# Performance work log

Measured on AMD Instinct MI355X. Metric: run time of the kernel, lower is better.

## Reference

```python
import jax, jax.numpy as jnp
import numpy as np

N, F_IN, D, R, E = 50000, 128, 96, 2, 800000


def setup_inputs() -> dict:
    key = jax.random.key(0)
    ks = jax.random.split(key, 8)
    sc = lambda k, shape: jax.random.normal(k, shape, jnp.float32) * 0.05
    return {
        "x": jax.random.normal(ks[0], (N, F_IN), jnp.float32),
        "edge_index": jax.random.randint(ks[1], (2, E), 0, N),
        "edge_attr": jax.random.uniform(ks[2], (E, R), dtype=jnp.float32),
        # nn.Linear(F_IN, D)
        "Wf": sc(ks[3], (D, F_IN)),
        "bf": jnp.zeros((D,), jnp.float32),
        # RGCNConv: per-relation weights, root weight, bias
        "W": sc(ks[4], (R, D, D)),
        "root": sc(ks[5], (D, D)),
        "bias": jnp.zeros((D,), jnp.float32),
    }


def _rgcn_conv(h, src, dst, etype, W, root, bias):
    # PyG RGCNConv (no bases/blocks, aggr='mean'):
    #   out = x @ root + bias + sum_r mean_{edges of type r}(x[src]) @ W[r]
    msg = h[src]  # [E, D] gather
    out = h @ root + bias
    for r in range(R):
        w = (etype == r).astype(h.dtype)[:, None]  # [E, 1] relation mask
        s = jax.ops.segment_sum(msg * w, dst, num_segments=N)   # [N, D] scatter-add
        cnt = jax.ops.segment_sum(w, dst, num_segments=N)       # [N, 1]
        agg = s / jnp.maximum(cnt, 1.0)                          # mean, safe for deg 0
        out = out + agg @ W[r]
    return out


def reference(x, edge_index, edge_attr, Wf, bf, W, root, bias):
    src, dst = edge_index[0], edge_index[1]
    etype = jnp.argmax(edge_attr, axis=1)  # [E]
    h = jax.nn.relu(x @ Wf.T + bf)
    for _ in range(3):
        h = jax.nn.relu(_rgcn_conv(h, src, dst, etype, W, root, bias))
    return h
```

## Files before the change

kernel.cpp:

```cpp
#include <hip/hip_runtime.h>

#define DN 96
#define FIN 128

typedef unsigned int uint_t;
typedef unsigned short ushort_t;

typedef __attribute__((ext_vector_type(8))) short short8v;
typedef __attribute__((ext_vector_type(4))) float f32x4;

#define MFMA16 __builtin_amdgcn_mfma_f32_16x16x32_bf16

struct __align__(4) U3 { uint_t x, y, z; };

__device__ __forceinline__ ushort_t f2bf(float f) {
    uint_t u = __float_as_uint(f);
    uint_t r = (u + 0x7FFFu + ((u >> 16) & 1u)) >> 16;
    return (ushort_t)r;
}
__device__ __forceinline__ float bf2f(ushort_t h) { return __uint_as_float(((uint_t)h) << 16); }
__device__ __forceinline__ float bf_lo(uint_t u) { return __uint_as_float(u << 16); }
__device__ __forceinline__ float bf_hi(uint_t u) { return __uint_as_float(u & 0xFFFF0000u); }

__device__ __forceinline__ U3 ldrow(const uint_t* __restrict__ g, int idx, int j) {
    return *(const U3*)(g + (size_t)idx * 48 + 3 * j);
}
__device__ __forceinline__ void acc6(float* s, U3 v) {
    s[0] += bf_lo(v.x); s[1] += bf_hi(v.x);
    s[2] += bf_lo(v.y); s[3] += bf_hi(v.y);
    s[4] += bf_lo(v.z); s[5] += bf_hi(v.z);
}


__global__ void hist_kernel(const int* __restrict__ ei, const float* __restrict__ ea,
                            int* __restrict__ cnt, uint2* __restrict__ kd, int E, int N) {
    int e = blockIdx.x * 256 + threadIdx.x;
    if (e >= E) return;
    int src = ei[e];
    int dst = ei[E + e];
    int r = (ea[2 * e + 1] > ea[2 * e]) ? 1 : 0;
    kd[e] = make_uint2((uint_t)dst | ((uint_t)r << 16), (uint_t)src);
    atomicAdd(&cnt[r * N + dst], 1);
}

__global__ void offsets_kernel(const int* __restrict__ cnt, int* __restrict__ total,
                               int* __restrict__ rowstart, int* __restrict__ fillptr,
                               int nbins) {
    __shared__ int sd[256];
    __shared__ int sbase;
    int t = threadIdx.x;
    int b = blockIdx.x * 256 + t;
    int v = (b < nbins) ? cnt[b] : 0;
    sd[t] = v;
    __syncthreads();
    for (int off = 1; off < 256; off <<= 1) {
        int add = (t >= off) ? sd[t - off] : 0;
        __syncthreads();
        sd[t] += add;
        __syncthreads();
    }
    if (t == 255) sbase = atomicAdd(total, sd[255]);
    __syncthreads();
    if (b < nbins) {
        int s = sbase + sd[t] - v;
        rowstart[b] = s;
        fillptr[b] = s;
    }
}


__global__ __launch_bounds__(256) void fill_part(const uint2* __restrict__ kd,
                            int* __restrict__ fillptr, int* __restrict__ srcs,
                            int E, int N, int PS) {
    int p = blockIdx.x & 7;
    int c = blockIdx.x >> 3;
    int base = c * 2048 + threadIdx.x;
#pragma unroll
    for (int i = 0; i < 8; i++) {
        int e = base + i * 256;
        if (e < E) {
            uint2 v = kd[e];
            int dst = v.x & 0xFFFF;
            if (dst / PS == p) {
                int r = (v.x >> 16) & 1;
                int pos = atomicAdd(&fillptr[r * N + dst], 1);
                srcs[pos] = (int)v.y;
            }
        }
    }
}


__global__ void init_zrow(ushort_t* g0A, ushort_t* g1A, ushort_t* g0B, ushort_t* g1B, int N) {
    int t = threadIdx.x;
    ushort_t* g = (blockIdx.x == 0) ? g0A : (blockIdx.x == 1) ? g1A
                 : (blockIdx.x == 2) ? g0B : g1B;
    g[(size_t)N * DN + t] = 0;
}


__global__ void pack_all(const float* __restrict__ root, const float* __restrict__ W,
                         const float* __restrict__ Wf,
                         ushort_t* __restrict__ Bph, ushort_t* __restrict__ Bpl,
                         ushort_t* __restrict__ Wfh, ushort_t* __restrict__ Wfl) {
    int l = threadIdx.x;
    int bid = blockIdx.x;
    if (bid < 54) {
        int fid = bid;
        int ct = fid / 3, ks = fid % 3;
        int mat = ct / 6, cw = ct % 6;
        const float* M = (mat == 0) ? root : (W + (size_t)(mat - 1) * DN * DN);
        int k0 = 32 * ks + (l >> 4) * 8;
        int col = 16 * cw + (l & 15);
#pragma unroll
        for (int j = 0; j < 8; j++) {
            float v = M[(size_t)(k0 + j) * DN + col];
            ushort_t h = f2bf(v);
            size_t idx = ((size_t)fid * 64 + l) * 8 + j;
            Bph[idx] = h;
            Bpl[idx] = f2bf(v - bf2f(h));
        }
    } else {
        int fid = bid - 54;
        int ct = fid >> 2, ks = fid & 3;
        int k0 = 32 * ks + (l >> 4) * 8;
        int col = 16 * ct + (l & 15);
#pragma unroll
        for (int j = 0; j < 8; j++) {
            float v = Wf[(size_t)col * FIN + k0 + j];
            ushort_t h = f2bf(v);
            size_t idx = ((size_t)fid * 64 + l) * 8 + j;
            Wfh[idx] = h;
            Wfl[idx] = f2bf(v - bf2f(h));
        }
    }
}


__device__ __forceinline__ void cvt8(float4 x, float4 y, short8v& hi, short8v& lo) {
    union { short8v v; ushort_t u[8]; } H, L;
    float f[8] = {x.x, x.y, x.z, x.w, y.x, y.y, y.z, y.w};
#pragma unroll
    for (int j = 0; j < 8; j++) {
        ushort_t h = f2bf(f[j]);
        H.u[j] = h;
        L.u[j] = f2bf(f[j] - bf2f(h));
    }
    hi = H.v; lo = L.v;
}


__global__ __launch_bounds__(256) void lin_gemm(
    const float* __restrict__ xin,
    const ushort_t* __restrict__ WfH, const ushort_t* __restrict__ WfL,
    const ushort_t* __restrict__ Bph, const ushort_t* __restrict__ Bpl,
    const float* __restrict__ bfv, const float* __restrict__ bias,
    float* __restrict__ hrootOut, ushort_t* __restrict__ g0Out, ushort_t* __restrict__ g1Out,
    int N)
{
    __shared__ float sout[4][16][100];
    int t = threadIdx.x;
    int l = t & 63;
    int w = t >> 6;

    int slab = blockIdx.x * 64 + w * 16;
    int row = slab + (l & 15);
    if (row >= N) row = N - 1;
    const float* xrow = xin + (size_t)row * FIN + ((l >> 4) * 8);
    short8v ah4[4], al4[4];
#pragma unroll
    for (int ks = 0; ks < 4; ks++) {
        float4 xa = *(const float4*)(xrow + 32 * ks);
        float4 xb = *(const float4*)(xrow + 32 * ks + 4);
        cvt8(xa, xb, ah4[ks], al4[ks]);
    }
#pragma unroll
    for (int ct = 0; ct < 6; ct++) {
        f32x4 hh = {0.f,0.f,0.f,0.f}, hl_ = {0.f,0.f,0.f,0.f}, lh = {0.f,0.f,0.f,0.f};
#pragma unroll
        for (int ks = 0; ks < 4; ks++) {
            size_t base = ((size_t)(ct * 4 + ks) * 64 + l) * 8;
            short8v bh = *(const short8v*)(WfH + base);
            short8v bl = *(const short8v*)(WfL + base);
            hh  = MFMA16(ah4[ks], bh, hh, 0, 0, 0);
            hl_ = MFMA16(ah4[ks], bl, hl_, 0, 0, 0);
            lh  = MFMA16(al4[ks], bh, lh, 0, 0, 0);
        }
        f32x4 acc = hh + hl_ + lh;
        int col = ct * 16 + (l & 15);
        float bv = bfv[col];
        int lr0 = (l >> 4) * 4;
#pragma unroll
        for (int r = 0; r < 4; r++) {
            float v = acc[r] + bv;
            sout[w][lr0 + r][col] = v > 0.f ? v : 0.f;
        }
    }
    __syncthreads();

    const float* srow = &sout[w][l & 15][0];
    int mbase = blockIdx.x * 64 + w * 16 + ((l >> 4) << 2);
    int k0 = (l >> 4) * 8;
    short8v ah[3], al[3];
#pragma unroll
    for (int ks = 0; ks < 3; ks++) {
        float4 xa = *(const float4*)(srow + k0 + 32 * ks);
        float4 xb = *(const float4*)(srow + k0 + 32 * ks + 4);
        cvt8(xa, xb, ah[ks], al[ks]);
    }
    for (int ct = 0; ct < 18; ct++) {
        f32x4 hh = {0.f,0.f,0.f,0.f}, hl_ = {0.f,0.f,0.f,0.f}, lh = {0.f,0.f,0.f,0.f};
#pragma unroll
        for (int ks = 0; ks < 3; ks++) {
            size_t base = ((size_t)(ct * 3 + ks) * 64 + l) * 8;
            short8v bh = *(const short8v*)(Bph + base);
            short8v bl = *(const short8v*)(Bpl + base);
            hh  = MFMA16(ah[ks], bh, hh, 0, 0, 0);
            hl_ = MFMA16(ah[ks], bl, hl_, 0, 0, 0);
            lh  = MFMA16(al[ks], bh, lh, 0, 0, 0);
        }
        f32x4 acc = hh + hl_ + lh;
        int mat = ct / 6;
        int col = (ct % 6) * 16 + (l & 15);
        if (mat == 0) {
            float bv = bias[col];
#pragma unroll
            for (int r = 0; r < 4; r++) {
                int m = mbase + r;
                if (m < N) hrootOut[(size_t)m * DN + col] = acc[r] + bv;
            }
        } else {
            ushort_t* g = (mat == 1) ? g0Out : g1Out;
#pragma unroll
            for (int r = 0; r < 4; r++) {
                int m = mbase + r;
                if (m < N) g[(size_t)m * DN + col] = f2bf(acc[r]);
            }
        }
    }
}


template <int GEMM>
__global__ __launch_bounds__(256) void layer_kernel(
    const float* __restrict__ hrootIn,
    const uint_t* __restrict__ g0In, const uint_t* __restrict__ g1In,
    const int* __restrict__ rowstart, const int* __restrict__ cnt,
    const int* __restrict__ srcs,
    const ushort_t* __restrict__ Bph, const ushort_t* __restrict__ Bpl,
    const float* __restrict__ bias,
    float* __restrict__ hrootOut, ushort_t* __restrict__ g0Out, ushort_t* __restrict__ g1Out,
    float* __restrict__ dout, int N)
{
    __shared__ float sout[16][100];
    int t = threadIdx.x;

    {
        int grp = t >> 4;
        int j = t & 15;
        int n = blockIdx.x * 16 + grp;
        bool valid = n < N;
        int nc = valid ? n : N - 1;

        const float* hr = hrootIn + (size_t)nc * DN + 6 * j;
        float2 p0 = *(const float2*)hr;
        float2 p1 = *(const float2*)(hr + 2);
        float2 p2 = *(const float2*)(hr + 4);

        float a[6] = {0.f,0.f,0.f,0.f,0.f,0.f};
#pragma unroll
        for (int r = 0; r < 2; r++) {
            int c    = valid ? cnt[r * N + nc] : 0;
            int base = valid ? rowstart[r * N + nc] : 0;
            const uint_t* g = r ? g1In : g0In;
            const int* sp = srcs + base;
            float sA[6] = {0.f,0.f,0.f,0.f,0.f,0.f};
            float sB[6] = {0.f,0.f,0.f,0.f,0.f,0.f};
            for (int e = 0; e < c; e += 8) {
                int i0 = (e + 0 < c) ? sp[e + 0] : N;
                int i1 = (e + 1 < c) ? sp[e + 1] : N;
                int i2 = (e + 2 < c) ? sp[e + 2] : N;
                int i3 = (e + 3 < c) ? sp[e + 3] : N;
                int i4 = (e + 4 < c) ? sp[e + 4] : N;
                int i5 = (e + 5 < c) ? sp[e + 5] : N;
                int i6 = (e + 6 < c) ? sp[e + 6] : N;
                int i7 = (e + 7 < c) ? sp[e + 7] : N;
                U3 v0 = ldrow(g, i0, j);
                U3 v1 = ldrow(g, i1, j);
                U3 v2 = ldrow(g, i2, j);
                U3 v3 = ldrow(g, i3, j);
                U3 v4 = ldrow(g, i4, j);
                U3 v5 = ldrow(g, i5, j);
                U3 v6 = ldrow(g, i6, j);
                U3 v7 = ldrow(g, i7, j);
                acc6(sA, v0); acc6(sB, v1); acc6(sA, v2); acc6(sB, v3);
                acc6(sA, v4); acc6(sB, v5); acc6(sA, v6); acc6(sB, v7);
            }
            float inv = (c > 0) ? 1.f / (float)c : 0.f;
#pragma unroll
            for (int k = 0; k < 6; k++) a[k] += (sA[k] + sB[k]) * inv;
        }
        float o0 = fmaxf(p0.x + a[0], 0.f);
        float o1 = fmaxf(p0.y + a[1], 0.f);
        float o2 = fmaxf(p1.x + a[2], 0.f);
        float o3 = fmaxf(p1.y + a[3], 0.f);
        float o4 = fmaxf(p2.x + a[4], 0.f);
        float o5 = fmaxf(p2.y + a[5], 0.f);
        if constexpr (GEMM) {
            float* dr = &sout[grp][6 * j];
            dr[0]=o0; dr[1]=o1; dr[2]=o2; dr[3]=o3; dr[4]=o4; dr[5]=o5;
        } else {
            if (valid) {
                float* dr = dout + (size_t)n * DN + 6 * j;
                *(float2*)(dr)     = make_float2(o0, o1);
                *(float2*)(dr + 2) = make_float2(o2, o3);
                *(float2*)(dr + 4) = make_float2(o4, o5);
            }
        }
    }

    if constexpr (!GEMM) return;
    __syncthreads();

    {
        int l = t & 63;
        int w = t >> 6;
        const float* srow = &sout[l & 15][0];
        int mbase = blockIdx.x * 16 + ((l >> 4) << 2);
        int k0 = (l >> 4) * 8;
        short8v ah[3], al[3];
#pragma unroll
        for (int ks = 0; ks < 3; ks++) {
            float4 xa = *(const float4*)(srow + k0 + 32 * ks);
            float4 xb = *(const float4*)(srow + k0 + 32 * ks + 4);
            cvt8(xa, xb, ah[ks], al[ks]);
        }
        int ctS, ctC;
        ctS = (w < 2) ? 5 * w : 10 + 4 * (w - 2);
        ctC = (w < 2) ? 5 : 4;
        for (int ci = 0; ci < ctC; ci++) {
            int ct = ctS + ci;
            f32x4 hh = {0.f,0.f,0.f,0.f}, hl_ = {0.f,0.f,0.f,0.f}, lh = {0.f,0.f,0.f,0.f};
#pragma unroll
            for (int ks = 0; ks < 3; ks++) {
                size_t base = ((size_t)(ct * 3 + ks) * 64 + l) * 8;
                short8v bh = *(const short8v*)(Bph + base);
                short8v bl = *(const short8v*)(Bpl + base);
                hh  = MFMA16(ah[ks], bh, hh, 0, 0, 0);
                hl_ = MFMA16(ah[ks], bl, hl_, 0, 0, 0);
                lh  = MFMA16(al[ks], bh, lh, 0, 0, 0);
            }
            f32x4 acc = hh + hl_ + lh;
            int mat = ct / 6;
            int col = (ct % 6) * 16 + (l & 15);
            if (mat == 0) {
                float bv = bias[col];
#pragma unroll
                for (int r = 0; r < 4; r++) {
                    int m = mbase + r;
                    if (m < N) hrootOut[(size_t)m * DN + col] = acc[r] + bv;
                }
            } else {
                ushort_t* g = (mat == 1) ? g0Out : g1Out;
#pragma unroll
                for (int r = 0; r < 4; r++) {
                    int m = mbase + r;
                    if (m < N) g[(size_t)m * DN + col] = f2bf(acc[r]);
                }
            }
        }
    }
}

extern "C" void kernel_launch(void* const* d_in, const int* in_sizes, int n_in,
                              void* d_out, int out_size, void* d_ws, size_t ws_size,
                              hipStream_t stream) {
    const float* x    = (const float*)d_in[0];
    const int*   ei   = (const int*)d_in[1];
    const float* ea   = (const float*)d_in[2];
    const float* Wf   = (const float*)d_in[3];
    const float* bf   = (const float*)d_in[4];
    const float* W    = (const float*)d_in[5];
    const float* root = (const float*)d_in[6];
    const float* bias = (const float*)d_in[7];
    float* out = (float*)d_out;

    int N = in_sizes[0] / FIN;
    int E = in_sizes[1] / 2;
    int nbins = 2 * N;
    int PS = (N + 7) / 8;
    size_t NR = (size_t)(N + 1) * DN;

    int* cnt      = (int*)d_ws;
    int* total    = cnt + nbins;
    int* rowstart = cnt + nbins + 4;
    int* fillptr  = rowstart + nbins;
    int* srcs     = fillptr + nbins;
    uint2* kd     = (uint2*)(srcs + E);
    ushort_t* Bph = (ushort_t*)(kd + E);
    ushort_t* Bpl = Bph + 54 * 512;
    ushort_t* Wfh = Bpl + 54 * 512;
    ushort_t* Wfl = Wfh + 24 * 512;
    float* hrootA = (float*)(Wfl + 24 * 512);
    ushort_t* g0A = (ushort_t*)(hrootA + (size_t)N * DN);
    ushort_t* g1A = g0A + NR;
    float* hrootB = (float*)(g1A + NR);
    ushort_t* g0B = (ushort_t*)(hrootB + (size_t)N * DN);
    ushort_t* g1B = g0B + NR;

    hipMemsetAsync(cnt, 0, (size_t)(nbins + 1) * sizeof(int), stream);

    hist_kernel<<<(E + 255) / 256, 256, 0, stream>>>(ei, ea, cnt, kd, E, N);
    offsets_kernel<<<(nbins + 255) / 256, 256, 0, stream>>>(cnt, total, rowstart, fillptr, nbins);
    int nchunk = (E + 2047) / 2048;
    fill_part<<<nchunk * 8, 256, 0, stream>>>(kd, fillptr, srcs, E, N, PS);
    pack_all<<<78, 64, 0, stream>>>(root, W, Wf, Bph, Bpl, Wfh, Wfl);
    init_zrow<<<4, 96, 0, stream>>>(g0A, g1A, g0B, g1B, N);

    int blk64 = (N + 63) / 64;
    int blk16 = (N + 15) / 16;

    lin_gemm<<<blk64, 256, 0, stream>>>(
        x, Wfh, Wfl, Bph, Bpl, bf, bias, hrootA, g0A, g1A, N);
    layer_kernel<1><<<blk16, 256, 0, stream>>>(
        hrootA, (const uint_t*)g0A, (const uint_t*)g1A, rowstart, cnt, srcs,
        Bph, Bpl, bias, hrootB, g0B, g1B, nullptr, N);
    layer_kernel<1><<<blk16, 256, 0, stream>>>(
        hrootB, (const uint_t*)g0B, (const uint_t*)g1B, rowstart, cnt, srcs,
        Bph, Bpl, bias, hrootA, g0A, g1A, nullptr, N);
    layer_kernel<0><<<blk16, 256, 0, stream>>>(
        hrootA, (const uint_t*)g0A, (const uint_t*)g1A, rowstart, cnt, srcs,
        nullptr, nullptr, nullptr, nullptr, nullptr, nullptr, out, N);
}
```

Measured before the change: 296.1 us.

## Merge preprocessing kernels and overlap CSR fill with the input linear GEMM

Edge decoding, weight packing and zero-row init now run in one prep kernel, so there are fewer launches. The per-destination histogram moves into a separate partitioned pass, where each block only counts destinations in its own slice. This is meant to improve atomic locality, at the cost of reading the edge keys once more. The CSR fill blocks and the first linear GEMM blocks now share one launch so the two can overlap. Edge keys are stored as two separate uint arrays (SoA) instead of uint2.

```diff
diff --git a/kernel.cpp b/kernel.cpp
--- a/kernel.cpp
+++ b/kernel.cpp
@@ -32,15 +32,86 @@
 }
 
 
-__global__ void hist_kernel(const int* __restrict__ ei, const float* __restrict__ ea,
-                            int* __restrict__ cnt, uint2* __restrict__ kd, int E, int N) {
-    int e = blockIdx.x * 256 + threadIdx.x;
-    if (e >= E) return;
-    int src = ei[e];
-    int dst = ei[E + e];
-    int r = (ea[2 * e + 1] > ea[2 * e]) ? 1 : 0;
-    kd[e] = make_uint2((uint_t)dst | ((uint_t)r << 16), (uint_t)src);
-    atomicAdd(&cnt[r * N + dst], 1);
+__global__ __launch_bounds__(256) void prep_kernel(
+    const int* __restrict__ ei, const float* __restrict__ ea,
+    uint_t* __restrict__ kdx, uint_t* __restrict__ kdy,
+    const float* __restrict__ root, const float* __restrict__ W, const float* __restrict__ Wf,
+    ushort_t* __restrict__ Bph, ushort_t* __restrict__ Bpl,
+    ushort_t* __restrict__ Wfh, ushort_t* __restrict__ Wfl,
+    ushort_t* g0A, ushort_t* g1A, ushort_t* g0B, ushort_t* g1B,
+    int E, int N, int KD_BLKS)
+{
+    int bid = blockIdx.x;
+    int t = threadIdx.x;
+    if (bid < KD_BLKS) {
+        int e = bid * 256 + t;
+        if (e < E) {
+            int src = ei[e];
+            int dst = ei[E + e];
+            float2 a = *(const float2*)(ea + 2 * e);
+            int r = (a.y > a.x) ? 1 : 0;
+            kdx[e] = (uint_t)dst | ((uint_t)r << 16);
+            kdy[e] = (uint_t)src;
+        }
+    } else if (bid < KD_BLKS + 78) {
+        if (t >= 64) return;
+        int l = t;
+        int fid = bid - KD_BLKS;
+        if (fid < 54) {
+            int ct = fid / 3, ks = fid % 3;
+            int mat = ct / 6, cw = ct % 6;
+            const float* M = (mat == 0) ? root : (W + (size_t)(mat - 1) * DN * DN);
+            int k0 = 32 * ks + (l >> 4) * 8;
+            int col = 16 * cw + (l & 15);
+#pragma unroll
+            for (int j = 0; j < 8; j++) {
+                float v = M[(size_t)(k0 + j) * DN + col];
+                ushort_t h = f2bf(v);
+                size_t idx = ((size_t)fid * 64 + l) * 8 + j;
+                Bph[idx] = h;
+                Bpl[idx] = f2bf(v - bf2f(h));
+            }
+        } else {
+            int f2 = fid - 54;
+            int ct = f2 >> 2, ks = f2 & 3;
+            int k0 = 32 * ks + (l >> 4) * 8;
+            int col = 16 * ct + (l & 15);
+#pragma unroll
+            for (int j = 0; j < 8; j++) {
+                float v = Wf[(size_t)col * FIN + k0 + j];
+                ushort_t h = f2bf(v);
+                size_t idx = ((size_t)f2 * 64 + l) * 8 + j;
+                Wfh[idx] = h;
+                Wfl[idx] = f2bf(v - bf2f(h));
+            }
+        }
+    } else {
+        int pair = bid - (KD_BLKS + 78);
+        ushort_t* ga = pair ? g0B : g0A;
+        ushort_t* gb = pair ? g1B : g1A;
+        if (t < 96) ga[(size_t)N * DN + t] = 0;
+        else if (t < 192) gb[(size_t)N * DN + (t - 96)] = 0;
+    }
+}
+
+
+__global__ __launch_bounds__(256) void hist_part(const uint_t* __restrict__ kdx,
+                                                 int* __restrict__ cnt, int E, int N, int PS) {
+    int p = blockIdx.x & 7;
+    int c = blockIdx.x >> 3;
+    int base = c * 2048 + threadIdx.x;
+#pragma unroll
+    for (int i = 0; i < 8; i++) {
+        int e = base + i * 256;
+        if (e < E) {
+            uint_t v = kdx[e];
+            int dst = v & 0xFFFF;
+            if (dst / PS == p) {
+                int r = (v >> 16) & 1;
+                atomicAdd(&cnt[r * N + dst], 1);
+            }
+        }
+    }
 }
 
 __global__ void offsets_kernel(const int* __restrict__ cnt, int* __restrict__ total,
@@ -69,74 +140,6 @@
 }
 
 
-__global__ __launch_bounds__(256) void fill_part(const uint2* __restrict__ kd,
-                            int* __restrict__ fillptr, int* __restrict__ srcs,
-                            int E, int N, int PS) {
-    int p = blockIdx.x & 7;
-    int c = blockIdx.x >> 3;
-    int base = c * 2048 + threadIdx.x;
-#pragma unroll
-    for (int i = 0; i < 8; i++) {
-        int e = base + i * 256;
-        if (e < E) {
-            uint2 v = kd[e];
-            int dst = v.x & 0xFFFF;
-            if (dst / PS == p) {
-                int r = (v.x >> 16) & 1;
-                int pos = atomicAdd(&fillptr[r * N + dst], 1);
-                srcs[pos] = (int)v.y;
-            }
-        }
-    }
-}
-
-
-__global__ void init_zrow(ushort_t* g0A, ushort_t* g1A, ushort_t* g0B, ushort_t* g1B, int N) {
-    int t = threadIdx.x;
-    ushort_t* g = (blockIdx.x == 0) ? g0A : (blockIdx.x == 1) ? g1A
-                 : (blockIdx.x == 2) ? g0B : g1B;
-    g[(size_t)N * DN + t] = 0;
-}
-
-
-__global__ void pack_all(const float* __restrict__ root, const float* __restrict__ W,
-                         const float* __restrict__ Wf,
-                         ushort_t* __restrict__ Bph, ushort_t* __restrict__ Bpl,
-                         ushort_t* __restrict__ Wfh, ushort_t* __restrict__ Wfl) {
-    int l = threadIdx.x;
-    int bid = blockIdx.x;
-    if (bid < 54) {
-        int fid = bid;
-        int ct = fid / 3, ks = fid % 3;
-        int mat = ct / 6, cw = ct % 6;
-        const float* M = (mat == 0) ? root : (W + (size_t)(mat - 1) * DN * DN);
-        int k0 = 32 * ks + (l >> 4) * 8;
-        int col = 16 * cw + (l & 15);
-#pragma unroll
-        for (int j = 0; j < 8; j++) {
-            float v = M[(size_t)(k0 + j) * DN + col];
-            ushort_t h = f2bf(v);
-            size_t idx = ((size_t)fid * 64 + l) * 8 + j;
-            Bph[idx] = h;
-            Bpl[idx] = f2bf(v - bf2f(h));
-        }
-    } else {
-        int fid = bid - 54;
-        int ct = fid >> 2, ks = fid & 3;
-        int k0 = 32 * ks + (l >> 4) * 8;
-        int col = 16 * ct + (l & 15);
-#pragma unroll
-        for (int j = 0; j < 8; j++) {
-            float v = Wf[(size_t)col * FIN + k0 + j];
-            ushort_t h = f2bf(v);
-            size_t idx = ((size_t)fid * 64 + l) * 8 + j;
-            Wfh[idx] = h;
-            Wfl[idx] = f2bf(v - bf2f(h));
-        }
-    }
-}
-
-
 __device__ __forceinline__ void cvt8(float4 x, float4 y, short8v& hi, short8v& lo) {
     union { short8v v; ushort_t u[8]; } H, L;
     float f[8] = {x.x, x.y, x.z, x.w, y.x, y.y, y.z, y.w};
@@ -150,20 +153,44 @@
 }
 
 
-__global__ __launch_bounds__(256) void lin_gemm(
+__global__ __launch_bounds__(256) void fill_lin(
+    const uint_t* __restrict__ kdx, const uint_t* __restrict__ kdy,
+    int* __restrict__ fillptr, int* __restrict__ srcs,
     const float* __restrict__ xin,
     const ushort_t* __restrict__ WfH, const ushort_t* __restrict__ WfL,
     const ushort_t* __restrict__ Bph, const ushort_t* __restrict__ Bpl,
     const float* __restrict__ bfv, const float* __restrict__ bias,
     float* __restrict__ hrootOut, ushort_t* __restrict__ g0Out, ushort_t* __restrict__ g1Out,
-    int N)
+    int E, int N, int PS, int FILL_BLKS)
 {
     __shared__ float sout[4][16][100];
     int t = threadIdx.x;
+
+    if (blockIdx.x < FILL_BLKS) {
+        int p = blockIdx.x & 7;
+        int c = blockIdx.x >> 3;
+        int base = c * 2048 + t;
+#pragma unroll
+        for (int i = 0; i < 8; i++) {
+            int e = base + i * 256;
+            if (e < E) {
+                uint_t v = kdx[e];
+                int dst = v & 0xFFFF;
+                if (dst / PS == p) {
+                    int r = (v >> 16) & 1;
+                    int pos = atomicAdd(&fillptr[r * N + dst], 1);
+                    srcs[pos] = (int)kdy[e];
+                }
+            }
+        }
+        return;
+    }
+
+    int bid2 = blockIdx.x - FILL_BLKS;
     int l = t & 63;
     int w = t >> 6;
 
-    int slab = blockIdx.x * 64 + w * 16;
+    int slab = bid2 * 64 + w * 16;
     int row = slab + (l & 15);
     if (row >= N) row = N - 1;
     const float* xrow = xin + (size_t)row * FIN + ((l >> 4) * 8);
@@ -199,7 +226,7 @@
     __syncthreads();
 
     const float* srow = &sout[w][l & 15][0];
-    int mbase = blockIdx.x * 64 + w * 16 + ((l >> 4) << 2);
+    int mbase = bid2 * 64 + w * 16 + ((l >> 4) << 2);
     int k0 = (l >> 4) * 8;
     short8v ah[3], al[3];
 #pragma unroll
@@ -396,8 +423,9 @@
     int* rowstart = cnt + nbins + 4;
     int* fillptr  = rowstart + nbins;
     int* srcs     = fillptr + nbins;
-    uint2* kd     = (uint2*)(srcs + E);
-    ushort_t* Bph = (ushort_t*)(kd + E);
+    uint_t* kdx   = (uint_t*)(srcs + E);
+    uint_t* kdy   = kdx + E;
+    ushort_t* Bph = (ushort_t*)(kdy + E);
     ushort_t* Bpl = Bph + 54 * 512;
     ushort_t* Wfh = Bpl + 54 * 512;
     ushort_t* Wfl = Wfh + 24 * 512;
@@ -410,18 +438,20 @@
 
     hipMemsetAsync(cnt, 0, (size_t)(nbins + 1) * sizeof(int), stream);
 
-    hist_kernel<<<(E + 255) / 256, 256, 0, stream>>>(ei, ea, cnt, kd, E, N);
-    offsets_kernel<<<(nbins + 255) / 256, 256, 0, stream>>>(cnt, total, rowstart, fillptr, nbins);
+    int KD_BLKS = (E + 255) / 256;
     int nchunk = (E + 2047) / 2048;
-    fill_part<<<nchunk * 8, 256, 0, stream>>>(kd, fillptr, srcs, E, N, PS);
-    pack_all<<<78, 64, 0, stream>>>(root, W, Wf, Bph, Bpl, Wfh, Wfl);
-    init_zrow<<<4, 96, 0, stream>>>(g0A, g1A, g0B, g1B, N);
-
+    int FILL_BLKS = nchunk * 8;
     int blk64 = (N + 63) / 64;
     int blk16 = (N + 15) / 16;
 
-    lin_gemm<<<blk64, 256, 0, stream>>>(
-        x, Wfh, Wfl, Bph, Bpl, bf, bias, hrootA, g0A, g1A, N);
+    prep_kernel<<<KD_BLKS + 78 + 2, 256, 0, stream>>>(
+        ei, ea, kdx, kdy, root, W, Wf, Bph, Bpl, Wfh, Wfl,
+        g0A, g1A, g0B, g1B, E, N, KD_BLKS);
+    hist_part<<<FILL_BLKS, 256, 0, stream>>>(kdx, cnt, E, N, PS);
+    offsets_kernel<<<(nbins + 255) / 256, 256, 0, stream>>>(cnt, total, rowstart, fillptr, nbins);
+    fill_lin<<<FILL_BLKS + blk64, 256, 0, stream>>>(
+        kdx, kdy, fillptr, srcs, x, Wfh, Wfl, Bph, Bpl, bf, bias,
+        hrootA, g0A, g1A, E, N, PS, FILL_BLKS);
     layer_kernel<1><<<blk16, 256, 0, stream>>>(
         hrootA, (const uint_t*)g0A, (const uint_t*)g1A, rowstart, cnt, srcs,
         Bph, Bpl, bias, hrootB, g0B, g1B, nullptr, N);
```

New measurement: 278.9 us. 1.06x faster.
